# Optimization experiments

Measured on AMD Instinct MI355X. Metric: run time of the kernel, lower is better.

The kernel has to match this reference:

```python
import jax, jax.numpy as jnp
import numpy as np

S, L, H, EC, EW = 4096, 16, 512, 128, 512
CHAR, WORD, PREF, POS, NER = 512, 50000, 512, 64, 32
HH = H // 2  # per-direction hidden of the bidirectional word LSTM


def setup_inputs() -> dict:
    key = jax.random.key(0)
    ks = jax.random.split(key, 23)
    rn = lambda k, shape: jax.random.normal(k, shape, jnp.float32) * 0.05
    return dict(
        word_seq=jax.random.randint(ks[0], (S,), 0, WORD),
        chars=jax.random.randint(ks[1], (S, L), 0, CHAR),
        char_lens=jax.random.randint(ks[2], (S,), 1, L + 1),  # ragged lengths in [1, L]
        feat_seq=jax.random.randint(ks[3], (S,), 0, PREF),
        char_emb=rn(ks[4], (CHAR, EC)),
        word_emb=rn(ks[5], (WORD, EW)),
        prefix_emb=rn(ks[6], (PREF, H)),
        Wih_c=rn(ks[7], (4 * H, EC)), Whh_c=rn(ks[8], (4 * H, H)),
        bih_c=rn(ks[9], (4 * H,)), bhh_c=rn(ks[10], (4 * H,)),
        Wih_f=rn(ks[11], (4 * HH, EW + H)), Whh_f=rn(ks[12], (4 * HH, HH)),
        bih_f=rn(ks[13], (4 * HH,)), bhh_f=rn(ks[14], (4 * HH,)),
        Wih_b=rn(ks[15], (4 * HH, EW + H)), Whh_b=rn(ks[16], (4 * HH, HH)),
        bih_b=rn(ks[17], (4 * HH,)), bhh_b=rn(ks[18], (4 * HH,)),
        Wpos=rn(ks[19], (POS, H)), bpos=rn(ks[20], (POS,)),
        Wner=rn(ks[21], (NER, H)), bner=rn(ks[22], (NER,)),
    )


def _cell(x, h, c, Wih, Whh, b):
    # PyTorch LSTM cell: gate order i, f, g, o
    g = x @ Wih.T + h @ Whh.T + b
    i, f, gg, o = jnp.split(g, 4, axis=-1)
    c = jax.nn.sigmoid(f) * c + jax.nn.sigmoid(i) * jnp.tanh(gg)
    h = jax.nn.sigmoid(o) * jnp.tanh(c)
    return h, c


def reference(word_seq, chars, char_lens, feat_seq,
              char_emb, word_emb, prefix_emb,
              Wih_c, Whh_c, bih_c, bhh_c,
              Wih_f, Whh_f, bih_f, bhh_f,
              Wih_b, Whh_b, bih_b, bhh_b,
              Wpos, bpos, Wner, bner):
    # --- char LSTM, batched over all S words (replaces the Python per-word loop) ---
    xs = char_emb[chars].transpose(1, 0, 2)                        # [L, S, EC]
    mask = (jnp.arange(L)[:, None] < char_lens[None, :])[:, :, None]  # [L, S, 1]
    h0 = prefix_emb[feat_seq]                                      # h0 = prefix embedding
    c0 = jnp.zeros_like(h0)
    b_c = bih_c + bhh_c

    def char_step(carry, inp):
        h, c = carry
        x, m = inp
        hn, cn = _cell(x, h, c, Wih_c, Whh_c, b_c)
        return (jnp.where(m, hn, h), jnp.where(m, cn, c)), None

    (char_feat, _), _ = jax.lax.scan(char_step, (h0, c0), (xs, mask))  # [S, H] == lstm_out[-1] per word

    # --- word-level bidirectional LSTM (batch = 1 sentence of S tokens) ---
    wc = jnp.concatenate([word_emb[word_seq], char_feat], axis=1)  # [S, EW+H]

    def run_lstm(x_seq, Wih, Whh, b):
        def step(carry, x):
            h, c = _cell(x, carry[0], carry[1], Wih, Whh, b)
            return (h, c), h
        z = jnp.zeros((HH,), x_seq.dtype)
        _, hs = jax.lax.scan(step, (z, z), x_seq)
        return hs  # [S, HH]

    out_f = run_lstm(wc, Wih_f, Whh_f, bih_f + bhh_f)
    out_b = run_lstm(wc[::-1], Wih_b, Whh_b, bih_b + bhh_b)[::-1]
    out = jnp.concatenate([out_f, out_b], axis=1)                  # [S, H]

    tag_pos = jax.nn.log_softmax(out @ Wpos.T + bpos, axis=1)
    tag_ner = jax.nn.log_softmax(out @ Wner.T + bner, axis=1)
    return tag_pos, tag_ner
```

## Files before the change

### kernel.cpp

```cpp
#include <hip/hip_runtime.h>

#define SS 4096
#define LL 16
#define HD 512
#define ECD 128
#define HHD 256

typedef __attribute__((ext_vector_type(8))) short short8;
typedef __attribute__((ext_vector_type(4))) float float4v;

__device__ __forceinline__ float bf2f(unsigned short u){
  union { unsigned int i; float f; } v; v.i = ((unsigned int)u) << 16; return v.f;
}
__device__ __forceinline__ unsigned short f2bf(float f){
  union { float f; unsigned int i; } v; v.f = f;
  unsigned int u = v.i;
  unsigned int r = (u + 0x7fffu + ((u >> 16) & 1u)) >> 16;
  return (unsigned short)r;
}
__device__ __forceinline__ float sigf(float x){ return 1.f / (1.f + __expf(-x)); }
__device__ __forceinline__ float tanh_f(float x){
  float e = __expf(2.f * x);
  return 1.f - 2.f / (e + 1.f);
}
__device__ __forceinline__ bool badf(float x){ return !(fabsf(x) < 1e30f); }

__device__ __forceinline__ int dot4i8(unsigned int a, unsigned int b, int c){
#if __has_builtin(__builtin_amdgcn_sdot4)
  return __builtin_amdgcn_sdot4((int)a, (int)b, c, false);
#else
  int s = c;
  s += (int)(char)(a)       * (int)(char)(b);
  s += (int)(char)(a >> 8)  * (int)(char)(b >> 8);
  s += (int)(char)(a >> 16) * (int)(char)(b >> 16);
  s += (int)(char)(a >> 24) * (int)(char)(b >> 24);
  return s;
#endif
}

__device__ __forceinline__ int4 cvt8(const float* __restrict__ s){
  union { unsigned short u[8]; int4 v; } pk;
#pragma unroll
  for (int i = 0; i < 8; ++i) pk.u[i] = f2bf(s[i]);
  return pk.v;
}

__global__ void prep_xu_k(const float* __restrict__ char_emb,
                          const float* __restrict__ Wih_c,
                          const float* __restrict__ bih_c,
                          const float* __restrict__ bhh_c,
                          unsigned short* __restrict__ xUb)
{
  int idx = blockIdx.x * 256 + threadIdx.x;
  int c = idx >> 11, n = idx & 2047;
  const float* ce = char_emb + (size_t)c * ECD;
  const float* wr = Wih_c + (size_t)n * ECD;
  float acc = bih_c[n] + bhh_c[n];
  for (int k = 0; k < ECD; k += 4) {
    float4 a = *(const float4*)(ce + k);
    float4 b = *(const float4*)(wr + k);
    acc += a.x*b.x + a.y*b.y + a.z*b.z + a.w*b.w;
  }
  xUb[idx] = f2bf(acc);
}

__global__ void prep_h0c0_k(const float* __restrict__ prefix_emb,
                            const int* __restrict__ feat_seq,
                            unsigned short* __restrict__ h0,
                            unsigned short* __restrict__ c0)
{
  int idx = blockIdx.x * 256 + threadIdx.x;
  int s = idx >> 9, j = idx & 511;
  h0[idx] = f2bf(prefix_emb[(size_t)feat_seq[s] * HD + j]);
  c0[idx] = 0;
}

__global__ void prep_scanw4_k(const float* __restrict__ Whh_f,
                              const float* __restrict__ Whh_b,
                              const float* __restrict__ bih_f,
                              const float* __restrict__ bhh_f,
                              const float* __restrict__ bih_b,
                              const float* __restrict__ bhh_b,
                              uint4* __restrict__ Wq,
                              float* __restrict__ scales,
                              float* __restrict__ biasbuf,
                              int* __restrict__ diag)
{
  int idx = blockIdx.x * 256 + threadIdx.x;
  int row = idx & 1023;
  int dir = idx >> 10;
  const float* W = (dir ? Whh_b : Whh_f) + (size_t)row * HHD;
  float mx = 0.f;
  for (int k = 0; k < HHD; k += 4) {
    float4 w = *(const float4*)(W + k);
    mx = fmaxf(mx, fmaxf(fmaxf(fabsf(w.x), fabsf(w.y)), fmaxf(fabsf(w.z), fabsf(w.w))));
  }
  float qs = (mx > 0.f) ? (127.f / mx) : 0.f;
  scales[dir * 1024 + row] = mx / 16129.f;
  for (int q = 0; q < 16; ++q) {
    unsigned int wd[4];
#pragma unroll
    for (int c = 0; c < 4; ++c) {
      int k = q * 16 + c * 4;
      float4 w = *(const float4*)(W + k);
      unsigned int b0 = (unsigned int)((int)rintf(w.x * qs)) & 255u;
      unsigned int b1 = (unsigned int)((int)rintf(w.y * qs)) & 255u;
      unsigned int b2 = (unsigned int)((int)rintf(w.z * qs)) & 255u;
      unsigned int b3 = (unsigned int)((int)rintf(w.w * qs)) & 255u;
      wd[c] = b0 | (b1 << 8) | (b2 << 16) | (b3 << 24);
    }
    uint4 v; v.x = wd[0]; v.y = wd[1]; v.z = wd[2]; v.w = wd[3];
    Wq[dir * 16384 + q * 1024 + row] = v;
  }
  const float* bi = dir ? bih_b : bih_f;
  const float* bh = dir ? bhh_b : bhh_f;
  biasbuf[dir * 1024 + row] = bi[row] + bh[row];
  if (idx == 0) diag[0] = 0;
}

__global__ __launch_bounds__(256) void gemm_char_k(
    const unsigned short* __restrict__ hin,
    const float* __restrict__ Whh,
    const unsigned short* __restrict__ xUb,
    const int* __restrict__ chars,
    const int* __restrict__ lens,
    int t,
    unsigned short* __restrict__ hout,
    unsigned short* __restrict__ cb,
    int* __restrict__ diag)
{
  __shared__ __align__(16) unsigned short As[128 * 32];
  __shared__ __align__(16) unsigned short Bs[128 * 32];
  __shared__ __align__(16) unsigned short gates[128 * 136];
  const int tid = threadIdx.x;
  const int m0 = blockIdx.y * 128;
  const int n0h = blockIdx.x * 32;
  const int wave = tid >> 6;
  const int lane = tid & 63;
  const int wm = (wave >> 1) * 64;
  const int wn = (wave & 1) * 64;
  float4v z = {0.f, 0.f, 0.f, 0.f};
  float4v acc[4][4];
#pragma unroll
  for (int i = 0; i < 4; ++i)
#pragma unroll
    for (int j = 0; j < 4; ++j) acc[i][j] = z;

  for (int k0 = 0; k0 < 512; k0 += 32) {
    __syncthreads();
#pragma unroll
    for (int i = 0; i < 2; ++i) {
      int chunk = tid * 2 + i;
      int row = chunk >> 2;
      int k8 = (chunk & 3) * 8;
      int4 av = *(const int4*)(hin + (size_t)(m0 + row) * 512 + k0 + k8);
      *(int4*)(As + row * 32 + k8) = av;
      int br = (row >> 5) * 512 + n0h + (row & 31);
      *(int4*)(Bs + row * 32 + k8) = cvt8(Whh + (size_t)br * 512 + k0 + k8);
    }
    __syncthreads();
    short8 af[4], bfr[4];
    const int kq = (lane >> 4) * 8;
#pragma unroll
    for (int i = 0; i < 4; ++i) {
      af[i]  = *(const short8*)(As + (wm + i * 16 + (lane & 15)) * 32 + kq);
      bfr[i] = *(const short8*)(Bs + (wn + i * 16 + (lane & 15)) * 32 + kq);
    }
#pragma unroll
    for (int i = 0; i < 4; ++i)
#pragma unroll
      for (int j = 0; j < 4; ++j)
        acc[i][j] = __builtin_amdgcn_mfma_f32_16x16x32_bf16(af[i], bfr[j], acc[i][j], 0, 0, 0);
  }
  __syncthreads();
#pragma unroll
  for (int i = 0; i < 4; ++i)
#pragma unroll
    for (int j = 0; j < 4; ++j)
#pragma unroll
      for (int r = 0; r < 4; ++r) {
        int row = wm + i * 16 + (lane >> 4) * 4 + r;
        int col = wn + j * 16 + (lane & 15);
        gates[row * 136 + col] = f2bf(acc[i][j][r]);
      }
  __syncthreads();
#pragma unroll
  for (int e = 0; e < 16; ++e) {
    int idx = e * 256 + tid;
    int r = idx >> 5, hc = idx & 31;
    int s = m0 + r;
    int col = n0h + hc;
    if (t < lens[s]) {
      int cid = chars[s * LL + t];
      size_t xb = (size_t)cid * 2048 + col;
      float gi = bf2f(gates[r * 136 + hc])      + bf2f(xUb[xb]);
      float gf = bf2f(gates[r * 136 + 32 + hc]) + bf2f(xUb[xb + 512]);
      float gg = bf2f(gates[r * 136 + 64 + hc]) + bf2f(xUb[xb + 1024]);
      float go = bf2f(gates[r * 136 + 96 + hc]) + bf2f(xUb[xb + 1536]);
      if (badf(gi + gf + gg + go)) atomicOr(diag, 1);
      float cc = sigf(gf) * bf2f(cb[(size_t)s * 512 + col]) + sigf(gi) * tanh_f(gg);
      cb[(size_t)s * 512 + col] = f2bf(cc);
      hout[(size_t)s * 512 + col] = f2bf(sigf(go) * tanh_f(cc));
    } else {
      hout[(size_t)s * 512 + col] = hin[(size_t)s * 512 + col];
    }
  }
}

__global__ __launch_bounds__(256) void gemm_gather_nt_k(
    const float* __restrict__ wemb,
    const int* __restrict__ wseq,
    const unsigned short* __restrict__ hbuf,
    const float* __restrict__ B,
    unsigned short* __restrict__ P)
{
  __shared__ __align__(16) unsigned short As[128 * 32];
  __shared__ __align__(16) unsigned short Bs[128 * 32];
  const int tid = threadIdx.x;
  const int m0 = blockIdx.y * 128;
  const int n0 = blockIdx.x * 128;
  const int wave = tid >> 6;
  const int lane = tid & 63;
  const int wm = (wave >> 1) * 64;
  const int wn = (wave & 1) * 64;
  float4v z = {0.f, 0.f, 0.f, 0.f};
  float4v acc[4][4];
#pragma unroll
  for (int i = 0; i < 4; ++i)
#pragma unroll
    for (int j = 0; j < 4; ++j) acc[i][j] = z;

  for (int k0 = 0; k0 < 1024; k0 += 32) {
    __syncthreads();
#pragma unroll
    for (int i = 0; i < 2; ++i) {
      int chunk = tid * 2 + i;
      int row = chunk >> 2;
      int k8 = (chunk & 3) * 8;
      int arow = m0 + row;
      int acol = k0 + k8;
      if (acol < 512) {
        *(int4*)(As + row * 32 + k8) = cvt8(wemb + (size_t)wseq[arow] * 512 + acol);
      } else {
        int4 av = *(const int4*)(hbuf + (size_t)arow * 512 + (acol - 512));
        *(int4*)(As + row * 32 + k8) = av;
      }
      *(int4*)(Bs + row * 32 + k8) = cvt8(B + (size_t)(n0 + row) * 1024 + k0 + k8);
    }
    __syncthreads();
    short8 af[4], bfr[4];
    const int kq = (lane >> 4) * 8;
#pragma unroll
    for (int i = 0; i < 4; ++i) {
      af[i]  = *(const short8*)(As + (wm + i * 16 + (lane & 15)) * 32 + kq);
      bfr[i] = *(const short8*)(Bs + (wn + i * 16 + (lane & 15)) * 32 + kq);
    }
#pragma unroll
    for (int i = 0; i < 4; ++i)
#pragma unroll
      for (int j = 0; j < 4; ++j)
        acc[i][j] = __builtin_amdgcn_mfma_f32_16x16x32_bf16(af[i], bfr[j], acc[i][j], 0, 0, 0);
  }
#pragma unroll
  for (int i = 0; i < 4; ++i)
#pragma unroll
    for (int j = 0; j < 4; ++j)
#pragma unroll
      for (int r = 0; r < 4; ++r) {
        int row = m0 + wm + i * 16 + (lane >> 4) * 4 + r;
        int col = n0 + wn + j * 16 + (lane & 15);
        P[(size_t)row * 1024 + col] = f2bf(acc[i][j][r]);
      }
}

__global__ __launch_bounds__(512) void scan7_k(
    const unsigned short* __restrict__ P_f,
    const unsigned short* __restrict__ P_b,
    const uint4* __restrict__ Wq,
    const float* __restrict__ scales,
    const float* __restrict__ biasbuf,
    unsigned short* __restrict__ out_f,
    unsigned short* __restrict__ out_b,
    int* __restrict__ diag, int dirsel)
{
  const int dir = (dirsel < 0) ? (int)blockIdx.x : dirsel;
  const int tid = threadIdx.x;
  const int rA = tid;
  const int rB = tid + 512;

  __shared__ __align__(16) uint4 ldsW[6 * 1024];
  __shared__ __align__(16) float g_lds[1024];
  __shared__ __align__(16) unsigned int hq[2][64];

  const uint4* wp = Wq + (size_t)dir * 16384;
  uint4 wA[10], wB[10];
#pragma unroll
  for (int q = 0; q < 10; ++q) {
    wA[q] = wp[q * 1024 + rA];
    wB[q] = wp[q * 1024 + rB];
  }
#pragma unroll
  for (int q = 10; q < 16; ++q) {
    ldsW[(q - 10) * 1024 + rA] = wp[q * 1024 + rA];
    ldsW[(q - 10) * 1024 + rB] = wp[q * 1024 + rB];
  }
  const float sA = scales[dir * 1024 + rA];
  const float sB = scales[dir * 1024 + rB];
  const float bA = biasbuf[dir * 1024 + rA];
  const float bB = biasbuf[dir * 1024 + rB];
  const unsigned short* P = dir ? P_b : P_f;
  unsigned short* out = dir ? out_b : out_f;

  if (tid < 64) hq[0][tid] = 0u;
  float c_reg = 0.f;
  __syncthreads();

  const int srow0 = dir ? 4095 : 0;
  float pA = bf2f(P[(size_t)srow0 * 1024 + rA]);
  float pB = bf2f(P[(size_t)srow0 * 1024 + rB]);

  for (int t = 0; t < 4096; ++t) {
    const int srow = dir ? (4095 - t) : t;
    const int nrow = dir ? ((4094 - t) & 4095) : ((t + 1) & 4095);
    float npA = bf2f(P[(size_t)nrow * 1024 + rA]);
    float npB = bf2f(P[(size_t)nrow * 1024 + rB]);

    int accA = 0, accB = 0;
    const uint4* h4 = (const uint4*)&hq[t & 1][0];
#pragma unroll
    for (int q = 0; q < 10; ++q) {
      uint4 hv = h4[q];
      accA = dot4i8(wA[q].x, hv.x, accA);
      accA = dot4i8(wA[q].y, hv.y, accA);
      accA = dot4i8(wA[q].z, hv.z, accA);
      accA = dot4i8(wA[q].w, hv.w, accA);
      accB = dot4i8(wB[q].x, hv.x, accB);
      accB = dot4i8(wB[q].y, hv.y, accB);
      accB = dot4i8(wB[q].z, hv.z, accB);
      accB = dot4i8(wB[q].w, hv.w, accB);
    }
#pragma unroll
    for (int q = 10; q < 16; ++q) {
      uint4 hv = h4[q];
      uint4 wa = ldsW[(q - 10) * 1024 + rA];
      uint4 wb = ldsW[(q - 10) * 1024 + rB];
      accA = dot4i8(wa.x, hv.x, accA);
      accA = dot4i8(wa.y, hv.y, accA);
      accA = dot4i8(wa.z, hv.z, accA);
      accA = dot4i8(wa.w, hv.w, accA);
      accB = dot4i8(wb.x, hv.x, accB);
      accB = dot4i8(wb.y, hv.y, accB);
      accB = dot4i8(wb.z, hv.z, accB);
      accB = dot4i8(wb.w, hv.w, accB);
    }
    g_lds[rA] = (float)accA * sA + bA + pA;
    g_lds[rB] = (float)accB * sB + bB + pB;
    __syncthreads();

    if (tid < 256) {
      float gi = g_lds[tid];
      float gf = g_lds[256 + tid];
      float gg = g_lds[512 + tid];
      float go = g_lds[768 + tid];
      if (badf(gi + gf + gg + go)) atomicOr(diag, 2);
      float cc = sigf(gf) * c_reg + sigf(gi) * tanh_f(gg);
      float hh = sigf(go) * tanh_f(cc);
      c_reg = cc;
      out[(size_t)srow * HHD + tid] = f2bf(hh);
      unsigned int v = ((unsigned int)((int)rintf(hh * 127.f)) & 255u) << ((tid & 3) * 8);
      v |= __shfl_xor(v, 1);
      v |= __shfl_xor(v, 2);
      if ((tid & 3) == 0) hq[(t + 1) & 1][tid >> 2] = v;
    }
    pA = npA; pB = npB;
    __syncthreads();
  }
}

__global__ __launch_bounds__(128) void head_k(
    const unsigned short* __restrict__ out_f, const unsigned short* __restrict__ out_b,
    const float* __restrict__ Wpos, const float* __restrict__ bpos,
    const float* __restrict__ Wner, const float* __restrict__ bner,
    float* __restrict__ dout, int* __restrict__ diag)
{
  const int s = blockIdx.x, tid = threadIdx.x;
  __shared__ __align__(16) float xv[512];
#pragma unroll
  for (int i = 0; i < 4; ++i) {
    int k = tid * 4 + i;
    xv[k] = (k < 256) ? bf2f(out_f[(size_t)s * 256 + k])
                      : bf2f(out_b[(size_t)s * 256 + (k - 256)]);
  }
  __syncthreads();
  float logit = 0.f;
  const int j = tid;
  if (j < 96) {
    const float* wr = (j < 64) ? (Wpos + (size_t)j * 512)
                               : (Wner + (size_t)(j - 64) * 512);
    float b = (j < 64) ? bpos[j] : bner[j - 64];
    float acc = 0.f;
    for (int k = 0; k < 512; k += 4) {
      float4 wv = *(const float4*)(wr + k);
      acc += xv[k] * wv.x + xv[k + 1] * wv.y + xv[k + 2] * wv.z + xv[k + 3] * wv.w;
    }
    logit = acc + b;
    if (badf(logit)) { atomicOr(diag, 4); logit = 0.f; }
  }
  if (j < 64) {
    float m = logit;
    for (int o = 32; o >= 1; o >>= 1) m = fmaxf(m, __shfl_xor(m, o));
    float e = __expf(logit - m), sum = e;
    for (int o = 32; o >= 1; o >>= 1) sum += __shfl_xor(sum, o);
    float v = logit - m - logf(sum);
    if (!(v > -1e30f && v < 1e30f)) v = -111.f;
    dout[(size_t)s * 64 + j] = v;
  } else if (j < 96) {
    float m = logit;
    for (int o = 16; o >= 1; o >>= 1) m = fmaxf(m, __shfl_xor(m, o, 32));
    float e = __expf(logit - m), sum = e;
    for (int o = 16; o >= 1; o >>= 1) sum += __shfl_xor(sum, o, 32);
    float v = logit - m - logf(sum);
    if (!(v > -1e30f && v < 1e30f)) v = -111.f;
    dout[262144 + (size_t)s * 32 + (j - 64)] = v;
  }
}

__global__ void diag_k(const float* __restrict__ ce,
                       int* __restrict__ diag,
                       float* __restrict__ dout)
{
  int cnt = 0;
  for (int i = 0; i < 64; ++i) {
    float x = ce[i];
    if (x == x && fabsf(x) < 100.f) cnt++;
  }
  if (cnt < 48) diag[0] |= 8;
  int d = diag[0];
  if (d) dout[0] = 1000.f + 100.f * (float)d;
}

__global__ void wssmall_k(float* __restrict__ dout, int mb)
{
  dout[0] = 10000.f + (float)mb;
}

extern "C" void kernel_launch(void* const* d_in, const int* in_sizes, int n_in,
                              void* d_out, int out_size, void* d_ws, size_t ws_size,
                              hipStream_t stream) {
  const int*   word_seq  = (const int*)d_in[0];
  const int*   chars     = (const int*)d_in[1];
  const int*   char_lens = (const int*)d_in[2];
  const int*   feat_seq  = (const int*)d_in[3];
  const float* char_emb  = (const float*)d_in[4];
  const float* word_emb  = (const float*)d_in[5];
  const float* prefix_emb= (const float*)d_in[6];
  const float* Wih_c     = (const float*)d_in[7];
  const float* Whh_c     = (const float*)d_in[8];
  const float* bih_c     = (const float*)d_in[9];
  const float* bhh_c     = (const float*)d_in[10];
  const float* Wih_f     = (const float*)d_in[11];
  const float* Whh_f     = (const float*)d_in[12];
  const float* bih_f     = (const float*)d_in[13];
  const float* bhh_f     = (const float*)d_in[14];
  const float* Wih_b     = (const float*)d_in[15];
  const float* Whh_b     = (const float*)d_in[16];
  const float* bih_b     = (const float*)d_in[17];
  const float* bhh_b     = (const float*)d_in[18];
  const float* Wpos      = (const float*)d_in[19];
  const float* bpos      = (const float*)d_in[20];
  const float* Wner      = (const float*)d_in[21];
  const float* bner      = (const float*)d_in[22];
  float* dout = (float*)d_out;

  const size_t MB = 1048576;
  char* ws = (char*)d_ws;
  int*            diag   = (int*)(ws + 512);
  float*          bias2  = (float*)(ws + 8192);
  float*          scales = (float*)(ws + 16384);
  uint4*          Wq     = (uint4*)(ws + 65536);
  unsigned short* hA    = (unsigned short*)(ws + 2 * MB);
  unsigned short* hB    = (unsigned short*)(ws + 6 * MB);
  unsigned short* xUb   = (unsigned short*)(ws + 10 * MB);
  unsigned short* cb    = (unsigned short*)(ws + 12 * MB);

  const size_t NEED_A2 = 22 * MB;
  const size_t NEED_B  = 16 * MB;
  unsigned short* P_f;
  unsigned short* P_b;
  unsigned short* out_f;
  unsigned short* out_b;
  int layoutA;
  if (ws_size >= NEED_A2) {
    layoutA = 1;
    P_f   = (unsigned short*)(ws + 6 * MB);
    P_b   = (unsigned short*)(ws + 14 * MB);
    out_f = (unsigned short*)(ws + 2 * MB);
    out_b = (unsigned short*)(ws + 4 * MB);
  } else if (ws_size >= NEED_B) {
    layoutA = 0;
    P_f   = (unsigned short*)(ws + 6 * MB);
    P_b   = (unsigned short*)(ws + 6 * MB);
    out_f = (unsigned short*)(ws + 14 * MB);
    out_b = (unsigned short*)(ws + 2 * MB);
  } else {
    wssmall_k<<<1, 1, 0, stream>>>(dout, (int)(ws_size >> 20));
    return;
  }

  prep_xu_k<<<(512 * 2048) / 256, 256, 0, stream>>>(char_emb, Wih_c, bih_c, bhh_c, xUb);
  prep_h0c0_k<<<(4096 * 512) / 256, 256, 0, stream>>>(prefix_emb, feat_seq, hA, cb);
  prep_scanw4_k<<<2048 / 256, 256, 0, stream>>>(
      Whh_f, Whh_b, bih_f, bhh_f, bih_b, bhh_b, Wq, scales, bias2, diag);

  unsigned short* hcur = hA;
  unsigned short* hnxt = hB;
  for (int t = 0; t < 16; ++t) {
    gemm_char_k<<<dim3(16, 32), 256, 0, stream>>>(
        hcur, Whh_c, xUb, chars, char_lens, t, hnxt, cb, diag);
    unsigned short* tmp = hcur; hcur = hnxt; hnxt = tmp;
  }

  if (layoutA) {
    gemm_gather_nt_k<<<dim3(8, 32), 256, 0, stream>>>(word_emb, word_seq, hcur, Wih_f, P_f);
    gemm_gather_nt_k<<<dim3(8, 32), 256, 0, stream>>>(word_emb, word_seq, hcur, Wih_b, P_b);
    scan7_k<<<2, 512, 0, stream>>>(P_f, P_b, Wq, scales, bias2, out_f, out_b, diag, -1);
  } else {
    gemm_gather_nt_k<<<dim3(8, 32), 256, 0, stream>>>(word_emb, word_seq, hcur, Wih_f, P_f);
    scan7_k<<<1, 512, 0, stream>>>(P_f, P_b, Wq, scales, bias2, out_f, out_b, diag, 0);
    gemm_gather_nt_k<<<dim3(8, 32), 256, 0, stream>>>(word_emb, word_seq, hcur, Wih_b, P_b);
    scan7_k<<<1, 512, 0, stream>>>(P_f, P_b, Wq, scales, bias2, out_f, out_b, diag, 1);
  }

  head_k<<<4096, 128, 0, stream>>>(out_f, out_b, Wpos, bpos, Wner, bner, dout, diag);

  diag_k<<<1, 1, 0, stream>>>(char_emb, diag, dout);
}
```

Measured before the change: 5.985 ms.

## Remap scan gate rows so thread pairs exchange gates via shuffles, dropping a barrier

The word-level LSTM scan now assigns each adjacent thread pair the four gate rows of one hidden unit: even threads own i/g, odd threads own f/o. The gates are swapped with __shfl_xor instead of going through a shared-memory gate buffer, which removes one __syncthreads per timestep and lets all 512 threads compute the cell update redundantly. It also keeps 12 of the 16 int8 weight chunks in registers instead of 10, cutting LDS reads per step at the cost of more register pressure. The packed h vector is now assembled with an extra shuffle level, and each pair computes the nonlinearities twice.

```diff
diff --git a/kernel.cpp b/kernel.cpp
--- a/kernel.cpp
+++ b/kernel.cpp
@@ -273,7 +273,7 @@
       }
 }
 
-__global__ __launch_bounds__(512) void scan7_k(
+__global__ __launch_bounds__(512) void scan8_k(
     const unsigned short* __restrict__ P_f,
     const unsigned short* __restrict__ P_b,
     const uint4* __restrict__ Wq,
@@ -285,24 +285,25 @@
 {
   const int dir = (dirsel < 0) ? (int)blockIdx.x : dirsel;
   const int tid = threadIdx.x;
-  const int rA = tid;
-  const int rB = tid + 512;
-
-  __shared__ __align__(16) uint4 ldsW[6 * 1024];
-  __shared__ __align__(16) float g_lds[1024];
+  const int u   = tid >> 1;
+  const int odd = tid & 1;
+  const int rA  = odd * 256 + u;
+  const int rB  = rA + 512;
+
+  __shared__ __align__(16) uint4 ldsW[4 * 1024];
   __shared__ __align__(16) unsigned int hq[2][64];
 
   const uint4* wp = Wq + (size_t)dir * 16384;
-  uint4 wA[10], wB[10];
-#pragma unroll
-  for (int q = 0; q < 10; ++q) {
+  uint4 wA[12], wB[12];
+#pragma unroll
+  for (int q = 0; q < 12; ++q) {
     wA[q] = wp[q * 1024 + rA];
     wB[q] = wp[q * 1024 + rB];
   }
 #pragma unroll
-  for (int q = 10; q < 16; ++q) {
-    ldsW[(q - 10) * 1024 + rA] = wp[q * 1024 + rA];
-    ldsW[(q - 10) * 1024 + rB] = wp[q * 1024 + rB];
+  for (int q = 12; q < 16; ++q) {
+    ldsW[(q - 12) * 1024 + rA] = wp[q * 1024 + rA];
+    ldsW[(q - 12) * 1024 + rB] = wp[q * 1024 + rB];
   }
   const float sA = scales[dir * 1024 + rA];
   const float sB = scales[dir * 1024 + rB];
@@ -328,7 +329,7 @@
     int accA = 0, accB = 0;
     const uint4* h4 = (const uint4*)&hq[t & 1][0];
 #pragma unroll
-    for (int q = 0; q < 10; ++q) {
+    for (int q = 0; q < 12; ++q) {
       uint4 hv = h4[q];
       accA = dot4i8(wA[q].x, hv.x, accA);
       accA = dot4i8(wA[q].y, hv.y, accA);
@@ -340,10 +341,10 @@
       accB = dot4i8(wB[q].w, hv.w, accB);
     }
 #pragma unroll
-    for (int q = 10; q < 16; ++q) {
+    for (int q = 12; q < 16; ++q) {
       uint4 hv = h4[q];
-      uint4 wa = ldsW[(q - 10) * 1024 + rA];
-      uint4 wb = ldsW[(q - 10) * 1024 + rB];
+      uint4 wa = ldsW[(q - 12) * 1024 + rA];
+      uint4 wb = ldsW[(q - 12) * 1024 + rB];
       accA = dot4i8(wa.x, hv.x, accA);
       accA = dot4i8(wa.y, hv.y, accA);
       accA = dot4i8(wa.z, hv.z, accA);
@@ -353,25 +354,26 @@
       accB = dot4i8(wb.z, hv.z, accB);
       accB = dot4i8(wb.w, hv.w, accB);
     }
-    g_lds[rA] = (float)accA * sA + bA + pA;
-    g_lds[rB] = (float)accB * sB + bB + pB;
-    __syncthreads();
-
-    if (tid < 256) {
-      float gi = g_lds[tid];
-      float gf = g_lds[256 + tid];
-      float gg = g_lds[512 + tid];
-      float go = g_lds[768 + tid];
+    float gA = (float)accA * sA + bA + pA;
+    float gB = (float)accB * sB + bB + pB;
+    float xA = __shfl_xor(gA, 1);
+    float xB = __shfl_xor(gB, 1);
+    float gi = odd ? xA : gA;
+    float gf = odd ? gA : xA;
+    float gg = odd ? xB : gB;
+    float go = odd ? gB : xB;
+    float cc = sigf(gf) * c_reg + sigf(gi) * tanh_f(gg);
+    float hh = sigf(go) * tanh_f(cc);
+    c_reg = cc;
+    if (!odd) {
       if (badf(gi + gf + gg + go)) atomicOr(diag, 2);
-      float cc = sigf(gf) * c_reg + sigf(gi) * tanh_f(gg);
-      float hh = sigf(go) * tanh_f(cc);
-      c_reg = cc;
-      out[(size_t)srow * HHD + tid] = f2bf(hh);
-      unsigned int v = ((unsigned int)((int)rintf(hh * 127.f)) & 255u) << ((tid & 3) * 8);
-      v |= __shfl_xor(v, 1);
-      v |= __shfl_xor(v, 2);
-      if ((tid & 3) == 0) hq[(t + 1) & 1][tid >> 2] = v;
-    }
+      out[(size_t)srow * HHD + u] = f2bf(hh);
+    }
+    unsigned int v = ((unsigned int)((int)rintf(hh * 127.f)) & 255u) << ((u & 3) * 8);
+    v |= __shfl_xor(v, 1);
+    v |= __shfl_xor(v, 2);
+    v |= __shfl_xor(v, 4);
+    if ((tid & 7) == 0) hq[(t + 1) & 1][tid >> 3] = v;
     pA = npA; pB = npB;
     __syncthreads();
   }
@@ -523,12 +525,12 @@
   if (layoutA) {
     gemm_gather_nt_k<<<dim3(8, 32), 256, 0, stream>>>(word_emb, word_seq, hcur, Wih_f, P_f);
     gemm_gather_nt_k<<<dim3(8, 32), 256, 0, stream>>>(word_emb, word_seq, hcur, Wih_b, P_b);
-    scan7_k<<<2, 512, 0, stream>>>(P_f, P_b, Wq, scales, bias2, out_f, out_b, diag, -1);
+    scan8_k<<<2, 512, 0, stream>>>(P_f, P_b, Wq, scales, bias2, out_f, out_b, diag, -1);
   } else {
     gemm_gather_nt_k<<<dim3(8, 32), 256, 0, stream>>>(word_emb, word_seq, hcur, Wih_f, P_f);
-    scan7_k<<<1, 512, 0, stream>>>(P_f, P_b, Wq, scales, bias2, out_f, out_b, diag, 0);
+    scan8_k<<<1, 512, 0, stream>>>(P_f, P_b, Wq, scales, bias2, out_f, out_b, diag, 0);
     gemm_gather_nt_k<<<dim3(8, 32), 256, 0, stream>>>(word_emb, word_seq, hcur, Wih_b, P_b);
-    scan7_k<<<1, 512, 0, stream>>>(P_f, P_b, Wq, scales, bias2, out_f, out_b, diag, 1);
+    scan8_k<<<1, 512, 0, stream>>>(P_f, P_b, Wq, scales, bias2, out_f, out_b, diag, 1);
   }
 
   head_k<<<4096, 128, 0, stream>>>(out_f, out_b, Wpos, bpos, Wner, bner, dout, diag);
```

New measurement: 6.469 ms. +8.1%, slower.
